# Kernel optimization log

Measured on AMD Instinct MI355X. Metric: run time of the kernel, lower is better.

## Reference

```python
import jax, jax.numpy as jnp
import numpy as np
import math

DIM = 512
HEADS = 8          # dim // num_head_channels = 512 // 64
HEAD_CH = 64
GROUPS = 32        # guided-diffusion normalization() = GroupNorm(32, dim)
EPS = 1e-5
CROSS_DIM = 768


def setup_inputs() -> dict:
    key = jax.random.key(0)
    ks = jax.random.split(key, 8)
    B, C, Hs, Ws, L = 16, DIM, 32, 32, 77
    x = jax.random.normal(ks[0], (B, C, Hs, Ws), dtype=jnp.float32)
    c = jax.random.normal(ks[1], (B, CROSS_DIM, L), dtype=jnp.float32)
    # GroupNorm affine params
    gamma = jnp.ones((C,), jnp.float32)
    beta = jnp.zeros((C,), jnp.float32)
    # 1x1 conv weights stored as [out, in]
    w_qkv = jax.random.normal(ks[2], (3 * C, C), jnp.float32) / math.sqrt(C)
    b_qkv = jnp.zeros((3 * C,), jnp.float32)
    w_c = jax.random.normal(ks[3], (2 * C, CROSS_DIM), jnp.float32) / math.sqrt(CROSS_DIM)
    b_c = jnp.zeros((2 * C,), jnp.float32)
    # NOTE: original proj_out is zero-initialized (zero_module); we use small
    # random weights so the reference exercises non-trivial math end-to-end.
    w_p = jax.random.normal(ks[4], (C, C), jnp.float32) / math.sqrt(C)
    b_p = jnp.zeros((C,), jnp.float32)
    return {"x": x, "c": c, "gamma": gamma, "beta": beta,
            "w_qkv": w_qkv, "b_qkv": b_qkv, "w_c": w_c, "b_c": b_c,
            "w_p": w_p, "b_p": b_p}


def reference(x, c, gamma, beta, w_qkv, b_qkv, w_c, b_c, w_p, b_p):
    B, C, Hs, Ws = x.shape
    T = Hs * Ws
    xf = x.reshape(B, C, T)

    # GroupNorm(32) over (channels_per_group, spatial)
    xg = xf.reshape(B, GROUPS, C // GROUPS, T)
    mean = xg.mean(axis=(2, 3), keepdims=True)
    var = xg.var(axis=(2, 3), keepdims=True)
    xn = ((xg - mean) * jax.lax.rsqrt(var + EPS)).reshape(B, C, T)
    xn = xn * gamma[None, :, None] + beta[None, :, None]

    # qkv 1x1 conv: [B, 3C, T]
    qkv = jnp.einsum('oc,bct->bot', w_qkv, xn) + b_qkv[None, :, None]
    q, k, v = jnp.split(qkv, 3, axis=1)
    q = q.reshape(B, HEADS, HEAD_CH, T)
    k = k.reshape(B, HEADS, HEAD_CH, T)
    v = v.reshape(B, HEADS, HEAD_CH, T)

    # cross-attn cond kv: [B, 2C, L] -> concat on sequence axis
    ckv = jnp.einsum('oc,bcl->bol', w_c, c) + b_c[None, :, None]
    kc, vc = jnp.split(ckv, 2, axis=1)
    L = c.shape[-1]
    k = jnp.concatenate([k, kc.reshape(B, HEADS, HEAD_CH, L)], axis=-1)
    v = jnp.concatenate([v, vc.reshape(B, HEADS, HEAD_CH, L)], axis=-1)

    scale = 1.0 / math.sqrt(HEAD_CH)
    # scores [B, H, T, T+L]; scale applied inside softmax as in FusedSoftmaxMaybeApex
    logits = jnp.einsum('bhct,bhcs->bhts', q, k) * scale
    w = jax.nn.softmax(logits, axis=-1)
    a = jnp.einsum('bhts,bhcs->bhct', w, v).reshape(B, C, T)

    h = jnp.einsum('oc,bct->bot', w_p, a) + b_p[None, :, None]
    return (xf + h).reshape(B, C, Hs, Ws)
```

## Files before the change

kernel.cpp:

```cpp
#include <hip/hip_runtime.h>

#define B_   16
#define C_   512
#define T_   1024
#define H_   8
#define D_   64
#define G_   32
#define L_   77
#define S_   1101
#define SPAD 1152
#define NPAD 51
#define CD_  768
#define BT_  (B_*T_)
#define SROW 72
#define QSC  0.18033688011112042f

typedef __bf16 bf16x8 __attribute__((ext_vector_type(8)));
typedef float  f32x4  __attribute__((ext_vector_type(4)));

static __device__ __forceinline__ unsigned short f2bf(float f) {
    unsigned int u = __float_as_uint(f);
    u = (u + 0x7fffu + ((u >> 16) & 1u)) >> 16;
    return (unsigned short)u;
}

static __device__ __forceinline__ unsigned int pk_bf16(float a, float b) {
    unsigned int d;
    asm("v_cvt_pk_bf16_f32 %0, %1, %2" : "=v"(d) : "v"(a), "v"(b));
    return d;
}

static __device__ __forceinline__ void gload_lds16(const unsigned short* g,
                                                   unsigned short* l) {
    __builtin_amdgcn_global_load_lds(
        (const __attribute__((address_space(1))) unsigned int*)g,
        (__attribute__((address_space(3))) unsigned int*)l, 16, 0, 0);
}

__global__ __launch_bounds__(256) void prep_k(const float* __restrict__ x,
                                              float* __restrict__ stats,
                                              const float* __restrict__ w_qkv,
                                              const float* __restrict__ w_p,
                                              const float* __restrict__ w_c,
                                              const float* __restrict__ cin,
                                              unsigned short* __restrict__ wqkv_pk,
                                              unsigned short* __restrict__ wp_pk,
                                              unsigned short* __restrict__ wc_pk,
                                              unsigned short* __restrict__ cpk) {
    const int tid = threadIdx.x;
    if (blockIdx.x < 512) {
        const int bg = blockIdx.x;
        const float* p = x + (size_t)bg * 16384;
        float s = 0.f, s2 = 0.f;
        for (int i = tid; i < 16384; i += 256) {
            float v = p[i];
            s += v; s2 += v * v;
        }
        __shared__ float rs[256], rs2[256];
        rs[tid] = s; rs2[tid] = s2;
        __syncthreads();
        for (int off = 128; off > 0; off >>= 1) {
            if (tid < off) { rs[tid] += rs[tid + off]; rs2[tid] += rs2[tid + off]; }
            __syncthreads();
        }
        if (tid == 0) {
            float mean = rs[0] * (1.0f / 16384.0f);
            float var  = rs2[0] * (1.0f / 16384.0f) - mean * mean;
            stats[2 * bg]     = mean;
            stats[2 * bg + 1] = rsqrtf(var + 1e-5f);
        }
        return;
    }
    if (blockIdx.x < 1408) {
        const int cid = (blockIdx.x - 512) * 256 + tid;
        const float* src;
        unsigned short* dst;
        if (cid < 98304) {
            const int ml = cid & 127, k8 = (cid >> 7) & 7, kt = (cid >> 10) & 7, mt = cid >> 13;
            src = w_qkv + (size_t)(mt * 128 + ml) * 512 + kt * 64 + k8 * 8;
            dst = wqkv_pk + (size_t)cid * 8;
        } else if (cid < 131072) {
            const int c2 = cid - 98304;
            const int ml = c2 & 127, k8 = (c2 >> 7) & 7, kt = (c2 >> 10) & 7, mt = c2 >> 13;
            src = w_p + (size_t)(mt * 128 + ml) * 512 + kt * 64 + k8 * 8;
            dst = wp_pk + (size_t)c2 * 8;
        } else {
            const int c3 = cid - 131072;
            const int ml = c3 & 127, k8 = (c3 >> 7) & 7;
            const int ktmt = c3 >> 10;
            const int kt = ktmt % 12, mt = ktmt / 12;
            src = w_c + (size_t)(mt * 128 + ml) * 768 + kt * 64 + k8 * 8;
            dst = wc_pk + (size_t)c3 * 8;
        }
        const float4 v0 = *(const float4*)src, v1 = *(const float4*)(src + 4);
        unsigned short tmp[8];
        tmp[0] = f2bf(v0.x); tmp[1] = f2bf(v0.y); tmp[2] = f2bf(v0.z); tmp[3] = f2bf(v0.w);
        tmp[4] = f2bf(v1.x); tmp[5] = f2bf(v1.y); tmp[6] = f2bf(v1.z); tmp[7] = f2bf(v1.w);
        *(uint4*)dst = *(uint4*)tmp;
        return;
    }
    const int idx2 = blockIdx.x - 1408;
    const int kt = idx2 % 12, b = idx2 / 12;
#pragma unroll
    for (int it = 0; it < 4; it++) {
        const int idx = it * 256 + tid;
        const int k8 = idx >> 7, l = idx & 127;
        unsigned short tmp[8];
        const float* src = cin + ((size_t)b * CD_ + kt * 64 + k8 * 8) * L_ + l;
#pragma unroll
        for (int q = 0; q < 8; q++)
            tmp[q] = (l < L_) ? f2bf(src[(size_t)q * L_]) : (unsigned short)0;
        *(uint4*)&cpk[(size_t)b * 98304 + ((size_t)(kt * 8 + k8)) * 1024 + (size_t)l * 8] =
            *(uint4*)tmp;
    }
}

__global__ __launch_bounds__(256) void gn_apply_t(const float* __restrict__ x,
                                                  const float* __restrict__ stats,
                                                  const float* __restrict__ gamma,
                                                  const float* __restrict__ beta,
                                                  unsigned short* __restrict__ xnT) {
    const int t0 = blockIdx.x * 64, kt = blockIdx.y, b = blockIdx.z;
    const int c0 = kt * 64;
    const int tid = threadIdx.x;
    __shared__ float st[64][66];
#pragma unroll
    for (int it = 0; it < 4; it++) {
        const int fid = it * 256 + tid;
        const int ci = fid >> 4, t4 = (fid & 15) * 4;
        const int c = c0 + ci;
        const float4 xv = *(const float4*)&x[((size_t)(b * C_ + c) << 10) + t0 + t4];
        const int bg = b * G_ + (c >> 4);
        const float mean = stats[2 * bg], istd = stats[2 * bg + 1];
        const float gs = gamma[c] * istd, gb = beta[c] - mean * gs;
        st[t4 + 0][ci] = xv.x * gs + gb;
        st[t4 + 1][ci] = xv.y * gs + gb;
        st[t4 + 2][ci] = xv.z * gs + gb;
        st[t4 + 3][ci] = xv.w * gs + gb;
    }
    __syncthreads();
#pragma unroll
    for (int it = 0; it < 2; it++) {
        const int cid = it * 256 + tid;
        const int k8 = cid >> 6, tl = cid & 63;
        const int n = (b << 10) + t0 + tl;
        const int nt = n >> 7, nm = n & 127;
        unsigned short tmp[8];
        const float* src = &st[tl][k8 * 8];
#pragma unroll
        for (int q = 0; q < 8; q++) tmp[q] = f2bf(src[q]);
        *(uint4*)&xnT[(((size_t)nt * 8 + kt) * 8 + k8) * 1024 + (size_t)nm * 8] = *(uint4*)tmp;
    }
}

template<int MODE, int KT>
static __device__ __forceinline__ void mgemm_body(const unsigned short* __restrict__ Apk,
                                                  const unsigned short* __restrict__ Bpk,
                                                  const float* __restrict__ bias,
                                                  const float* __restrict__ resid,
                                                  unsigned short* __restrict__ qpk,
                                                  unsigned short* __restrict__ kpk,
                                                  unsigned short* __restrict__ vpk,
                                                  float* __restrict__ outp,
                                                  unsigned short* lds,
                                                  const int nt, const int mt, const int zz) {
    const int tid = threadIdx.x, wave = tid >> 6, lane = tid & 63;
    const int quad = lane >> 4, l16 = lane & 15;
    const int mw = (wave & 1) * 64, nw = (wave >> 1) * 64;

    f32x4 acc[4][4];
#pragma unroll
    for (int i = 0; i < 4; i++)
#pragma unroll
        for (int j = 0; j < 4; j++) acc[i][j] = (f32x4){0.f, 0.f, 0.f, 0.f};

    const unsigned short* Ab = Apk + (size_t)mt * KT * 8192;
    const unsigned short* Bb = Bpk + ((MODE == 2) ? (size_t)zz * KT * 8192 : 0)
                                   + (size_t)nt * KT * 8192;

    for (int kt = 0; kt < KT; kt++) {
        const unsigned short* as = Ab + kt * 8192 + wave * 2048 + lane * 8;
        const unsigned short* bs = Bb + kt * 8192 + wave * 2048 + lane * 8;
        unsigned short* la = lds + wave * 2048;
        unsigned short* lb = lds + 8192 + wave * 2048;
#pragma unroll
        for (int j = 0; j < 4; j++) {
            gload_lds16(as + j * 512, la + j * 512);
            gload_lds16(bs + j * 512, lb + j * 512);
        }
        __syncthreads();
#pragma unroll
        for (int kh = 0; kh < 2; kh++) {
            const int k8 = kh * 4 + quad;
            bf16x8 af[4], bfr[4];
#pragma unroll
            for (int i = 0; i < 4; i++) {
                af[i]  = *(const bf16x8*)&lds[(size_t)(k8 * 128 + mw + i * 16 + l16) * 8];
                bfr[i] = *(const bf16x8*)&lds[8192 + (size_t)(k8 * 128 + nw + i * 16 + l16) * 8];
            }
#pragma unroll
            for (int mi = 0; mi < 4; mi++)
#pragma unroll
                for (int ni = 0; ni < 4; ni++)
                    acc[mi][ni] = __builtin_amdgcn_mfma_f32_16x16x32_bf16(
                        af[mi], bfr[ni], acc[mi][ni], 0, 0, 0);
        }
        __syncthreads();
    }

    const int gm0 = mt * 128 + mw;
    const int gn0 = nt * 128 + nw;

    if (MODE == 1) {
        const int b = gn0 >> 10, t0 = gn0 & 1023;
#pragma unroll
        for (int mi = 0; mi < 4; mi++) {
#pragma unroll
            for (int r = 0; r < 4; r++) {
                const int m = gm0 + mi * 16 + quad * 4 + r;
                const float bv = bias[m];
                const size_t rowb = ((size_t)(b * C_ + m) << 10) + t0;
#pragma unroll
                for (int ni = 0; ni < 4; ni++) {
                    const size_t a = rowb + ni * 16 + l16;
                    outp[a] = acc[mi][ni][r] + bv + resid[a];
                }
            }
        }
        return;
    }

    const int region = gm0 >> 9;
    const int h = (gm0 & 511) >> 6;
    const int b = (MODE == 2) ? zz : (gn0 >> 10);
    const int bh = b * 8 + h;
    const bool vregion = (MODE == 0) ? (region == 2) : (region == 1);

    if (!vregion) {
        const float sc = (MODE == 0 && region == 0) ? QSC : 1.0f;
        unsigned short* base;
        int trow0;
        if (MODE == 0) {
            base = (region == 0) ? qpk + (size_t)bh * 16 * 4096
                                 : kpk + (size_t)bh * 18 * 4096;
            trow0 = gn0 & 1023;
        } else {
            base = kpk + (size_t)(bh * 18 + 16 + (gn0 >> 6)) * 4096;
            trow0 = -1;
        }
#pragma unroll
        for (int mi = 0; mi < 4; mi++) {
            const int k8 = mi * 2 + (quad >> 1);
            const int sub = (quad & 1) * 4;
#pragma unroll
            for (int ni = 0; ni < 4; ni++) {
                float vv[4];
                bool valid = true;
                if (MODE == 2) valid = (gn0 + ni * 16 + l16) < L_;
#pragma unroll
                for (int r = 0; r < 4; r++)
                    vv[r] = valid ? (acc[mi][ni][r] + bias[gm0 + mi * 16 + quad * 4 + r]) * sc
                                  : 0.f;
                uint2 d;
                d.x = pk_bf16(vv[0], vv[1]);
                d.y = pk_bf16(vv[2], vv[3]);
                unsigned short* dst;
                if (MODE == 0) {
                    const int t = trow0 + ni * 16 + l16;
                    dst = base + (size_t)(t >> 6) * 4096 + ((size_t)k8 * 64 + (t & 63)) * 8 + sub;
                } else {
                    const int row = ni * 16 + l16;
                    dst = base + ((size_t)k8 * 64 + row) * 8 + sub;
                }
                *(uint2*)dst = d;
            }
        }
    } else {
        unsigned short* wlds = lds + wave * 4608;
#pragma unroll
        for (int mi = 0; mi < 4; mi++)
#pragma unroll
            for (int ni = 0; ni < 4; ni++) {
                bool valid = true;
                if (MODE == 2) valid = (gn0 + ni * 16 + l16) < L_;
#pragma unroll
                for (int r = 0; r < 4; r++) {
                    const float v = valid ? acc[mi][ni][r] + bias[gm0 + mi * 16 + quad * 4 + r]
                                          : 0.f;
                    wlds[(mi * 16 + quad * 4 + r) * SROW + ni * 16 + l16] = f2bf(v);
                }
            }
        __syncthreads();
        const int stile = (MODE == 0) ? ((gn0 & 1023) >> 6) : (16 + (gn0 >> 6));
        unsigned short* dst = vpk + (size_t)(bh * 18 + stile) * 4096;
        const int sk8 = lane & 7, cb = lane >> 3;
#pragma unroll
        for (int it = 0; it < 8; it++) {
            const int ch = it * 8 + cb;
            *(uint4*)&dst[((size_t)sk8 * 64 + ch) * 8] =
                *(const uint4*)&wlds[ch * SROW + sk8 * 8];
        }
    }
}

__global__ __launch_bounds__(256) void mgemm_qkvc_k(const unsigned short* __restrict__ wqkv_pk,
                                                    const unsigned short* __restrict__ xnT,
                                                    const float* __restrict__ b_qkv,
                                                    const unsigned short* __restrict__ wc_pk,
                                                    const unsigned short* __restrict__ cpk,
                                                    const float* __restrict__ b_c,
                                                    unsigned short* __restrict__ qpk,
                                                    unsigned short* __restrict__ kpk,
                                                    unsigned short* __restrict__ vpk) {
    __shared__ unsigned short lds[18432];
    if (blockIdx.y < 12) {
        mgemm_body<0, 8>(wqkv_pk, xnT, b_qkv, nullptr, qpk, kpk, vpk, nullptr,
                         lds, blockIdx.x, blockIdx.y, 0);
    } else {
        mgemm_body<2, 12>(wc_pk, cpk, b_c, nullptr, nullptr, kpk, vpk, nullptr,
                          lds, 0, blockIdx.x & 7, blockIdx.x >> 3);
    }
}

__global__ __launch_bounds__(256) void mgemm_proj_k(const unsigned short* __restrict__ Apk,
                                                    const unsigned short* __restrict__ Bpk,
                                                    const float* __restrict__ bias,
                                                    const float* __restrict__ resid,
                                                    float* __restrict__ outp) {
    __shared__ unsigned short lds[18432];
    mgemm_body<1, 8>(Apk, Bpk, bias, resid, nullptr, nullptr, nullptr, outp,
                     lds, blockIdx.x, blockIdx.y, 0);
}

__global__ __launch_bounds__(256, 3) void flash_k(const unsigned short* __restrict__ qpk,
                                                  const unsigned short* __restrict__ kpk,
                                                  const unsigned short* __restrict__ vpk,
                                                  unsigned short* __restrict__ aT) {
    __shared__ __align__(16) unsigned short ks[2][4096];
    __shared__ __align__(16) unsigned short vs[2][4096];
    __shared__ __align__(16) unsigned short psA[4 * 32 * SROW];

    const int tid  = threadIdx.x;
    const int wave = tid >> 6, lane = tid & 63;
    const int quad = lane >> 4, l16 = lane & 15;
    const int bh  = blockIdx.x;
    const int b = bh >> 3, h = bh & 7;
    const int qt0 = blockIdx.y * 128;

    const unsigned short* qtb = qpk + ((size_t)bh * 16 + blockIdx.y * 2 + (wave >> 1)) * 4096;
    const int qr0 = (wave & 1) * 32 + l16;
    bf16x8 bq0[2], bq1[2];
#pragma unroll
    for (int s = 0; s < 2; s++) {
        bq0[s] = *(const bf16x8*)&qtb[((size_t)quad * 64 + qr0 + s * 16) * 8];
        bq1[s] = *(const bf16x8*)&qtb[((size_t)(quad + 4) * 64 + qr0 + s * 16) * 8];
    }

    unsigned short* ps = psA + wave * 32 * SROW;

    const unsigned short* kbase = kpk + (size_t)bh * 18 * 4096 + wave * 1024 + lane * 8;
    const unsigned short* vbase = vpk + (size_t)bh * 18 * 4096 + wave * 1024 + lane * 8;

#define STAGE(p, t) do {                                             \
        const unsigned short* kg = kbase + (size_t)(t) * 4096;       \
        const unsigned short* vg = vbase + (size_t)(t) * 4096;       \
        unsigned short* lkp = &ks[p][wave * 1024];                   \
        unsigned short* lvp = &vs[p][wave * 1024];                   \
        gload_lds16(kg, lkp);       gload_lds16(kg + 512, lkp + 512);\
        gload_lds16(vg, lvp);       gload_lds16(vg + 512, lvp + 512);\
    } while (0)

    float rsum[2] = {0.f, 0.f};
    f32x4 o_acc[2][4];
#pragma unroll
    for (int s = 0; s < 2; s++)
#pragma unroll
        for (int nb = 0; nb < 4; nb++) o_acc[s][nb] = (f32x4){0.f, 0.f, 0.f, 0.f};

    STAGE(0, 0);
    __syncthreads();

    for (int t = 0; t < 18; t++) {
        const int p = t & 1;
        if (t < 17) STAGE(p ^ 1, t + 1);
        const unsigned short* kb = &ks[p][0];
        const unsigned short* vb = &vs[p][0];

        f32x4 sacc[2][4];
        __builtin_amdgcn_s_setprio(1);
#pragma unroll
        for (int sb = 0; sb < 4; sb++) {
            const bf16x8 ak0 = *(const bf16x8*)&kb[((size_t)quad * 64 + sb * 16 + l16) * 8];
            const bf16x8 ak1 = *(const bf16x8*)&kb[((size_t)(quad + 4) * 64 + sb * 16 + l16) * 8];
#pragma unroll
            for (int s = 0; s < 2; s++) {
                f32x4 z = (f32x4){0.f, 0.f, 0.f, 0.f};
                z = __builtin_amdgcn_mfma_f32_16x16x32_bf16(ak0, bq0[s], z, 0, 0, 0);
                z = __builtin_amdgcn_mfma_f32_16x16x32_bf16(ak1, bq1[s], z, 0, 0, 0);
                sacc[s][sb] = z;
            }
        }
        __builtin_amdgcn_s_setprio(0);

#pragma unroll
        for (int s = 0; s < 2; s++) {
#pragma unroll
            for (int sb = 0; sb < 4; sb++) {
                const float e0 = __builtin_exp2f(sacc[s][sb][0]);
                const float e1 = __builtin_exp2f(sacc[s][sb][1]);
                const float e2 = __builtin_exp2f(sacc[s][sb][2]);
                const float e3 = __builtin_exp2f(sacc[s][sb][3]);
                rsum[s] += (e0 + e1) + (e2 + e3);
                uint2 d;
                d.x = pk_bf16(e0, e1);
                d.y = pk_bf16(e2, e3);
                *(uint2*)&ps[(s * 16 + l16) * SROW + sb * 16 + quad * 4] = d;
            }
        }
        asm volatile("s_waitcnt lgkmcnt(0)" ::: "memory");

        bf16x8 ap0[2], ap1[2];
#pragma unroll
        for (int s = 0; s < 2; s++) {
            ap0[s] = *(const bf16x8*)&ps[(s * 16 + l16) * SROW + quad * 8];
            ap1[s] = *(const bf16x8*)&ps[(s * 16 + l16) * SROW + 32 + quad * 8];
        }
        __builtin_amdgcn_s_setprio(1);
#pragma unroll
        for (int nb = 0; nb < 4; nb++) {
            const bf16x8 bv0 = *(const bf16x8*)&vb[((size_t)quad * 64 + nb * 16 + l16) * 8];
            const bf16x8 bv1 = *(const bf16x8*)&vb[((size_t)(quad + 4) * 64 + nb * 16 + l16) * 8];
#pragma unroll
            for (int s = 0; s < 2; s++) {
                o_acc[s][nb] = __builtin_amdgcn_mfma_f32_16x16x32_bf16(ap0[s], bv0, o_acc[s][nb], 0, 0, 0);
                o_acc[s][nb] = __builtin_amdgcn_mfma_f32_16x16x32_bf16(ap1[s], bv1, o_acc[s][nb], 0, 0, 0);
            }
        }
        __builtin_amdgcn_s_setprio(0);
        __syncthreads();
    }
#undef STAGE

    float linv[2][4];
#pragma unroll
    for (int s = 0; s < 2; s++) {
        float lsum = rsum[s];
        lsum += __shfl_xor(lsum, 16);
        lsum += __shfl_xor(lsum, 32);
#pragma unroll
        for (int r = 0; r < 4; r++) {
            const float lr = __shfl(lsum, quad * 4 + r);
            linv[s][r] = 1.0f / (lr - (float)NPAD);
        }
    }

#pragma unroll
    for (int s = 0; s < 2; s++)
#pragma unroll
        for (int nb = 0; nb < 4; nb++)
#pragma unroll
            for (int r = 0; r < 4; r++)
                ps[(s * 16 + quad * 4 + r) * SROW + nb * 16 + l16] =
                    f2bf(o_acc[s][nb][r] * linv[s][r]);
    asm volatile("s_waitcnt lgkmcnt(0)" ::: "memory");
    const int k8 = lane >> 3;
#pragma unroll
    for (int it = 0; it < 4; it++) {
        const int tl = (lane & 7) + it * 8;
        const int n = (b << 10) + qt0 + wave * 32 + tl;
        const int ntb = n >> 7, nm = n & 127;
        *(uint4*)&aT[(((size_t)ntb * 8 + h) * 8 + k8) * 1024 + (size_t)nm * 8] =
            *(const uint4*)&ps[tl * SROW + k8 * 8];
    }
}

extern "C" void kernel_launch(void* const* d_in, const int* in_sizes, int n_in,
                              void* d_out, int out_size, void* d_ws, size_t ws_size,
                              hipStream_t stream) {
    const float* x     = (const float*)d_in[0];
    const float* cin   = (const float*)d_in[1];
    const float* gamma = (const float*)d_in[2];
    const float* beta  = (const float*)d_in[3];
    const float* w_qkv = (const float*)d_in[4];
    const float* b_qkv = (const float*)d_in[5];
    const float* w_c   = (const float*)d_in[6];
    const float* b_c   = (const float*)d_in[7];
    const float* w_p   = (const float*)d_in[8];
    const float* b_p   = (const float*)d_in[9];
    float* out = (float*)d_out;

    float* ws    = (float*)d_ws;
    float* stats = ws;
    unsigned short* xnT     = (unsigned short*)(ws + 1024);
    unsigned short* wqkv_pk = xnT + 8388608;
    unsigned short* wp_pk   = wqkv_pk + 786432;
    unsigned short* wc_pk   = wp_pk + 262144;
    unsigned short* cpk     = wc_pk + 786432;
    unsigned short* qpk     = cpk + 1572864;
    unsigned short* kpk     = qpk + 8388608;
    unsigned short* vpk     = kpk + 9437184;
    unsigned short* aT      = vpk + 9437184;

    prep_k<<<dim3(1600), 256, 0, stream>>>(x, stats, w_qkv, w_p, w_c, cin,
                                           wqkv_pk, wp_pk, wc_pk, cpk);
    gn_apply_t<<<dim3(16, 8, 16), 256, 0, stream>>>(x, stats, gamma, beta, xnT);
    mgemm_qkvc_k<<<dim3(128, 13), 256, 0, stream>>>(wqkv_pk, xnT, b_qkv,
                                                    wc_pk, cpk, b_c,
                                                    qpk, kpk, vpk);
    flash_k<<<dim3(128, 8), 256, 0, stream>>>(qpk, kpk, vpk, aT);
    mgemm_proj_k<<<dim3(128, 4), 256, 0, stream>>>(wp_pk, aT, b_p, x, out);
}
```

Measured before the change: 273.1 us.

## Transpose softmax P tile in registers via permlane swaps instead of LDS

The flash attention kernel no longer writes the exponentiated score tile to LDS and reads it back in MFMA A-operand layout. It rearranges the packed bf16 values across lanes with v_permlane32/16_swap instructions, removing the LDS round trip and its waitcnt stall. Because the P scratch buffer is gone, the K/V double buffers and the epilogue scratch share one smaller LDS array, and launch bounds rise to 4 blocks per SM for occupancy. The s_setprio hints are also removed. Higher occupancy may add register pressure or spills.

```diff
diff --git a/kernel.cpp b/kernel.cpp
--- a/kernel.cpp
+++ b/kernel.cpp
@@ -17,6 +17,7 @@
 
 typedef __bf16 bf16x8 __attribute__((ext_vector_type(8)));
 typedef float  f32x4  __attribute__((ext_vector_type(4)));
+typedef unsigned int u32x4 __attribute__((ext_vector_type(4)));
 
 static __device__ __forceinline__ unsigned short f2bf(float f) {
     unsigned int u = __float_as_uint(f);
@@ -28,6 +29,13 @@
     unsigned int d;
     asm("v_cvt_pk_bf16_f32 %0, %1, %2" : "=v"(d) : "v"(a), "v"(b));
     return d;
+}
+
+static __device__ __forceinline__ void swap32(unsigned& a, unsigned& b) {
+    asm volatile("v_permlane32_swap_b32 %0, %1" : "+v"(a), "+v"(b));
+}
+static __device__ __forceinline__ void swap16(unsigned& a, unsigned& b) {
+    asm volatile("v_permlane16_swap_b32 %0, %1" : "+v"(a), "+v"(b));
 }
 
 static __device__ __forceinline__ void gload_lds16(const unsigned short* g,
@@ -332,13 +340,11 @@
                      lds, blockIdx.x, blockIdx.y, 0);
 }
 
-__global__ __launch_bounds__(256, 3) void flash_k(const unsigned short* __restrict__ qpk,
+__global__ __launch_bounds__(256, 4) void flash_k(const unsigned short* __restrict__ qpk,
                                                   const unsigned short* __restrict__ kpk,
                                                   const unsigned short* __restrict__ vpk,
                                                   unsigned short* __restrict__ aT) {
-    __shared__ __align__(16) unsigned short ks[2][4096];
-    __shared__ __align__(16) unsigned short vs[2][4096];
-    __shared__ __align__(16) unsigned short psA[4 * 32 * SROW];
+    __shared__ __align__(16) unsigned short smem[16384];
 
     const int tid  = threadIdx.x;
     const int wave = tid >> 6, lane = tid & 63;
@@ -356,18 +362,16 @@
         bq1[s] = *(const bf16x8*)&qtb[((size_t)(quad + 4) * 64 + qr0 + s * 16) * 8];
     }
 
-    unsigned short* ps = psA + wave * 32 * SROW;
-
     const unsigned short* kbase = kpk + (size_t)bh * 18 * 4096 + wave * 1024 + lane * 8;
     const unsigned short* vbase = vpk + (size_t)bh * 18 * 4096 + wave * 1024 + lane * 8;
 
-#define STAGE(p, t) do {                                             \
-        const unsigned short* kg = kbase + (size_t)(t) * 4096;       \
-        const unsigned short* vg = vbase + (size_t)(t) * 4096;       \
-        unsigned short* lkp = &ks[p][wave * 1024];                   \
-        unsigned short* lvp = &vs[p][wave * 1024];                   \
-        gload_lds16(kg, lkp);       gload_lds16(kg + 512, lkp + 512);\
-        gload_lds16(vg, lvp);       gload_lds16(vg + 512, lvp + 512);\
+#define STAGE(p, t) do {                                                  \
+        const unsigned short* kg = kbase + (size_t)(t) * 4096;            \
+        const unsigned short* vg = vbase + (size_t)(t) * 4096;            \
+        unsigned short* lkp = smem + (p) * 4096 + wave * 1024;            \
+        unsigned short* lvp = smem + 8192 + (p) * 4096 + wave * 1024;     \
+        gload_lds16(kg, lkp);       gload_lds16(kg + 512, lkp + 512);     \
+        gload_lds16(vg, lvp);       gload_lds16(vg + 512, lvp + 512);     \
     } while (0)
 
     float rsum[2] = {0.f, 0.f};
@@ -383,11 +387,10 @@
     for (int t = 0; t < 18; t++) {
         const int p = t & 1;
         if (t < 17) STAGE(p ^ 1, t + 1);
-        const unsigned short* kb = &ks[p][0];
-        const unsigned short* vb = &vs[p][0];
+        const unsigned short* kb = smem + p * 4096;
+        const unsigned short* vb = smem + 8192 + p * 4096;
 
         f32x4 sacc[2][4];
-        __builtin_amdgcn_s_setprio(1);
 #pragma unroll
         for (int sb = 0; sb < 4; sb++) {
             const bf16x8 ak0 = *(const bf16x8*)&kb[((size_t)quad * 64 + sb * 16 + l16) * 8];
@@ -400,10 +403,11 @@
                 sacc[s][sb] = z;
             }
         }
-        __builtin_amdgcn_s_setprio(0);
-
+
+        bf16x8 ap0[2], ap1[2];
 #pragma unroll
         for (int s = 0; s < 2; s++) {
+            unsigned w[4][2];
 #pragma unroll
             for (int sb = 0; sb < 4; sb++) {
                 const float e0 = __builtin_exp2f(sacc[s][sb][0]);
@@ -411,21 +415,20 @@
                 const float e2 = __builtin_exp2f(sacc[s][sb][2]);
                 const float e3 = __builtin_exp2f(sacc[s][sb][3]);
                 rsum[s] += (e0 + e1) + (e2 + e3);
-                uint2 d;
-                d.x = pk_bf16(e0, e1);
-                d.y = pk_bf16(e2, e3);
-                *(uint2*)&ps[(s * 16 + l16) * SROW + sb * 16 + quad * 4] = d;
-            }
-        }
-        asm volatile("s_waitcnt lgkmcnt(0)" ::: "memory");
-
-        bf16x8 ap0[2], ap1[2];
-#pragma unroll
-        for (int s = 0; s < 2; s++) {
-            ap0[s] = *(const bf16x8*)&ps[(s * 16 + l16) * SROW + quad * 8];
-            ap1[s] = *(const bf16x8*)&ps[(s * 16 + l16) * SROW + 32 + quad * 8];
-        }
-        __builtin_amdgcn_s_setprio(1);
+                w[sb][0] = pk_bf16(e0, e1);
+                w[sb][1] = pk_bf16(e2, e3);
+            }
+            swap32(w[0][0], w[1][0]); swap16(w[0][0], w[1][0]);
+            swap32(w[0][1], w[1][1]); swap16(w[0][1], w[1][1]);
+            swap32(w[2][0], w[3][0]); swap16(w[2][0], w[3][0]);
+            swap32(w[2][1], w[3][1]); swap16(w[2][1], w[3][1]);
+            union { u32x4 u; bf16x8 v; } c0, c1;
+            c0.u = (u32x4){w[0][0], w[0][1], w[1][0], w[1][1]};
+            c1.u = (u32x4){w[2][0], w[2][1], w[3][0], w[3][1]};
+            ap0[s] = c0.v;
+            ap1[s] = c1.v;
+        }
+
 #pragma unroll
         for (int nb = 0; nb < 4; nb++) {
             const bf16x8 bv0 = *(const bf16x8*)&vb[((size_t)quad * 64 + nb * 16 + l16) * 8];
@@ -436,7 +439,6 @@
                 o_acc[s][nb] = __builtin_amdgcn_mfma_f32_16x16x32_bf16(ap1[s], bv1, o_acc[s][nb], 0, 0, 0);
             }
         }
-        __builtin_amdgcn_s_setprio(0);
         __syncthreads();
     }
 #undef STAGE
@@ -454,6 +456,7 @@
         }
     }
 
+    unsigned short* ps = smem + wave * (32 * SROW);
 #pragma unroll
     for (int s = 0; s < 2; s++)
 #pragma unroll
```

Result: faster. 266.6 us (-2.4%).
